# Performance work log

Hardware: AMD Instinct MI355X
Metric: run time of the kernel (lower is better)

Reference implementation:

```python
import jax, jax.numpy as jnp
import numpy as np

B, T = 1, 2048
N_EMBD = 4096
N_HEAD = 32
N_GROUPS = 8
HEAD = 128
Q_PER_KV = N_HEAD // N_GROUPS  # 4
WINDOW = 1024
EPS = 1e-5
ROPE_THETA = 10000.0


def setup_inputs() -> dict:
    key = jax.random.key(0)
    k0, k1, k2 = jax.random.split(key, 3)
    x = jax.random.normal(k0, (B, T, N_EMBD), dtype=jnp.float32)
    # RoPE tables: cos/sin of shape [T, HEAD] (rotary_percentage=1.0)
    inv_freq = 1.0 / (ROPE_THETA ** (jnp.arange(0, HEAD, 2, dtype=jnp.float32) / HEAD))
    ang = jnp.arange(T, dtype=jnp.float32)[:, None] * inv_freq[None, :]  # [T, HEAD//2]
    ang = jnp.concatenate([ang, ang], axis=-1)  # [T, HEAD]
    cos, sin = jnp.cos(ang), jnp.sin(ang)
    qkv_out = (N_HEAD + 2 * N_GROUPS) * HEAD  # 6144
    W_qkv = jax.random.normal(k1, (qkv_out, N_EMBD), dtype=jnp.float32) * 0.02
    W_proj = jax.random.normal(k2, (N_EMBD, N_HEAD * HEAD), dtype=jnp.float32) * 0.02
    norm_q_w = jnp.ones((N_HEAD * HEAD,), dtype=jnp.float32)
    norm_k_w = jnp.ones((N_GROUPS * HEAD,), dtype=jnp.float32)
    return {"x": x, "cos": cos, "sin": sin, "W_qkv": W_qkv,
            "norm_q_w": norm_q_w, "norm_k_w": norm_k_w, "W_proj": W_proj}


def _rmsnorm(x, w):
    # RMSNorm over last dim, matching litgpt RMSNorm (eps inside sqrt)
    var = jnp.mean(x * x, axis=-1, keepdims=True)
    return x * jax.lax.rsqrt(var + EPS) * w


def _apply_rope(x, cos, sin):
    # x: [B, H, T, D]; cos/sin: [T, D] (broadcast over B, H)
    d = x.shape[-1]
    x1, x2 = x[..., : d // 2], x[..., d // 2:]
    rotated = jnp.concatenate([-x2, x1], axis=-1)
    return x * cos + rotated * sin


def reference(x, cos, sin, W_qkv, norm_q_w, norm_k_w, W_proj):
    Bx, Tx, _ = x.shape
    qkv = jnp.einsum('btc,oc->bto', x, W_qkv)  # [B, T, (H+2G)*D]
    q_size = N_HEAD * HEAD
    kv_size = N_GROUPS * HEAD
    q = qkv[..., :q_size]
    k = qkv[..., q_size:q_size + kv_size]
    v = qkv[..., q_size + kv_size:]
    # norm_qk: RMSNorm over the full flattened q / k dims (pre head reshape)
    q = _rmsnorm(q, norm_q_w)
    k = _rmsnorm(k, norm_k_w)
    q = q.reshape(Bx, Tx, N_HEAD, HEAD).transpose(0, 2, 1, 3)     # [B, H, T, D]
    k = k.reshape(Bx, Tx, N_GROUPS, HEAD).transpose(0, 2, 1, 3)   # [B, G, T, D]
    v = v.reshape(Bx, Tx, N_GROUPS, HEAD).transpose(0, 2, 1, 3)   # [B, G, T, D]
    # rope_n_elem == head_size (rotary_percentage = 1.0)
    q = _apply_rope(q, cos, sin)
    k = _apply_rope(k, cos, sin)
    # GQA: expand kv groups to heads (repeat_interleave on head dim)
    k = jnp.repeat(k, Q_PER_KV, axis=1)  # [B, H, T, D]
    v = jnp.repeat(v, Q_PER_KV, axis=1)
    scale = 1.0 / jnp.sqrt(jnp.float32(HEAD))  # attention_scores_scalar is None
    scores = jnp.einsum('bhqd,bhkd->bhqk', q, k) * scale
    # causal + sliding-window mask: allowed iff 0 <= q_idx - kv_idx < WINDOW
    d = jnp.arange(Tx)[:, None] - jnp.arange(Tx)[None, :]
    bias = jnp.where((d >= 0) & (d < WINDOW), 0.0, -jnp.inf).astype(scores.dtype)
    attn = jax.nn.softmax(scores + bias, axis=-1)
    y = jnp.einsum('bhqk,bhkd->bhqd', attn, v)        # [B, H, T, D]
    y = y.transpose(0, 2, 1, 3).reshape(Bx, Tx, N_HEAD * HEAD)
    return jnp.einsum('bth,oh->bto', y, W_proj)       # [B, T, n_embd]
```

## Files before the change

kernel.cpp:

```cpp
#include <hip/hip_runtime.h>
#include <stdint.h>
#include <stddef.h>

#define T_SEQ 2048
#define WINDOW_SZ 1024

typedef __attribute__((ext_vector_type(4))) float f32x4;
typedef __attribute__((ext_vector_type(16))) float f32x16;
typedef __attribute__((ext_vector_type(8))) short s16x8;
typedef __attribute__((ext_vector_type(4))) short s16x4;

__device__ inline unsigned short f2bf(float f) {
  union { float f; unsigned u; } v; v.f = f;
  unsigned u = v.u;
  return (unsigned short)((u + 0x7fffu + ((u >> 16) & 1u)) >> 16);
}
__device__ inline float bf2f(unsigned short u) {
  union { unsigned u; float f; } v; v.u = ((unsigned)u) << 16; return v.f;
}

__device__ inline void gld_lds16(const unsigned short* g, unsigned short* l) {
  __builtin_amdgcn_global_load_lds((const __attribute__((address_space(1))) void*)g,
                                   (__attribute__((address_space(3))) void*)l, 16, 0, 0);
}

__device__ inline void store_out(float* p, float v) { *p = v; }
__device__ inline void store_out(unsigned short* p, float v) { *p = f2bf(v); }

__global__ __launch_bounds__(256) void cvt_all(const float* __restrict__ x,
                                               const float* __restrict__ wqkv,
                                               const float* __restrict__ wproj,
                                               unsigned short* __restrict__ x_bf,
                                               unsigned short* __restrict__ wqkv_bf,
                                               unsigned short* __restrict__ wproj_bf) {
  int i = blockIdx.x * 256 + threadIdx.x;
  const float* s; unsigned short* d; int j;
  if (i < 2097152)       { s = x;     d = x_bf;     j = i; }
  else if (i < 8388608)  { s = wqkv;  d = wqkv_bf;  j = i - 2097152; }
  else                   { s = wproj; d = wproj_bf; j = i - 8388608; }
  float4 v = ((const float4*)s)[j];
  ushort4 o;
  o.x = f2bf(v.x); o.y = f2bf(v.y); o.z = f2bf(v.z); o.w = f2bf(v.w);
  ((ushort4*)d)[j] = o;
}

template <typename OutT>
__global__ __launch_bounds__(256) void gemm_bt(const unsigned short* __restrict__ A,
                                               const unsigned short* __restrict__ Bt,
                                               OutT* __restrict__ C, int M, int N, int K) {
  __shared__ unsigned short As[128 * 64];
  __shared__ unsigned short Bs[128 * 64];
  const int tid  = threadIdx.x;
  const int wave = tid >> 6, lane = tid & 63;
  const int l32 = lane & 31, khalf = lane >> 5;
  const int m0 = blockIdx.y << 7, n0 = blockIdx.x << 7;
  const int wr = (wave >> 1) << 6;
  const int wc = (wave & 1) << 6;
  const int srow = wave * 8 + (lane >> 3);
  const int gchunk0 = lane & 7;

  f32x16 acc[2][2] = {};

  for (int k0 = 0; k0 < K; k0 += 64) {
#pragma unroll
    for (int j = 0; j < 4; j++) {
      int r = j * 32 + srow;
      int gc = gchunk0 ^ (r & 7);
      gld_lds16(A  + (size_t)(m0 + r) * K + k0 + gc * 8, &As[(j * 32 + wave * 8) * 64]);
      gld_lds16(Bt + (size_t)(n0 + r) * K + k0 + gc * 8, &Bs[(j * 32 + wave * 8) * 64]);
    }
    __syncthreads();
#pragma unroll
    for (int s = 0; s < 4; s++) {
      s16x8 af[2], bfr[2];
      int chunk = s * 2 + khalf;
#pragma unroll
      for (int i = 0; i < 2; i++) {
        int ra = wr + i * 32 + l32;
        af[i]  = *(const s16x8*)&As[ra * 64 + ((chunk ^ (ra & 7)) * 8)];
        int rb = wc + i * 32 + l32;
        bfr[i] = *(const s16x8*)&Bs[rb * 64 + ((chunk ^ (rb & 7)) * 8)];
      }
#pragma unroll
      for (int mi = 0; mi < 2; mi++)
#pragma unroll
        for (int ni = 0; ni < 2; ni++)
          acc[mi][ni] = __builtin_amdgcn_mfma_f32_32x32x16_bf16(af[mi], bfr[ni], acc[mi][ni], 0, 0, 0);
    }
    __syncthreads();
  }
#pragma unroll
  for (int mi = 0; mi < 2; mi++)
#pragma unroll
    for (int ni = 0; ni < 2; ni++) {
      int col = n0 + wc + ni * 32 + l32;
      int rbase = m0 + wr + mi * 32 + 4 * khalf;
#pragma unroll
      for (int reg = 0; reg < 16; reg++) {
        int row = rbase + (reg & 3) + 8 * (reg >> 2);
        store_out(&C[(size_t)row * N + col], acc[mi][ni][reg]);
      }
    }
}

__device__ inline void stage_half(const unsigned short* __restrict__ g, int ldk,
                                  int grow0, int k0, unsigned short* lds,
                                  int wave, int lane) {
#pragma unroll
  for (int j = 0; j < 2; j++) {
    int rloc = j * 64 + wave * 8 + (lane >> 3);
    int lc = (lane & 7) ^ (rloc & 7);
    gld_lds16(g + (size_t)(grow0 + rloc) * ldk + k0 + lc * 8,
              lds + (j * 64 + wave * 8) * 64);
  }
}
__device__ inline void stage_64(const unsigned short* __restrict__ g, int ldk,
                                int grow0, int k0, unsigned short* lds,
                                int wave, int lane) {
  int rloc = wave * 8 + (lane >> 3);
  int lc = (lane & 7) ^ (rloc & 7);
  gld_lds16(g + (size_t)(grow0 + rloc) * ldk + k0 + lc * 8,
            lds + (wave * 8) * 64);
}

__global__ __launch_bounds__(512, 2) void gemm256(const unsigned short* __restrict__ A,
                                                  const unsigned short* __restrict__ Bt,
                                                  unsigned short* __restrict__ C,
                                                  int M, int N, int K) {
  __shared__ unsigned short S[57344];
  const int tid = threadIdx.x, wave = tid >> 6, lane = tid & 63;
  const int quad = lane >> 4, l16 = lane & 15;
  const int wm = wave >> 2, wn = wave & 3;
  const int m0 = blockIdx.y << 8, n0 = blockIdx.x * 192;
  const int NT = K >> 6;

  f32x4 acc[8][3] = {};

  stage_half(Bt, K, n0,       0, &S[16384],        wave, lane);
  stage_64  (Bt, K, n0 + 128, 0, &S[16384 + 8192], wave, lane);
  stage_half(A,  K, m0,       0, &S[0],            wave, lane);
  stage_half(A,  K, m0 + 128, 0, &S[8192],         wave, lane);
  if (NT > 1) {
    stage_half(Bt, K, n0,       64, &S[28672 + 16384],        wave, lane);
    stage_64  (Bt, K, n0 + 128, 64, &S[28672 + 16384 + 8192], wave, lane);
  }
  asm volatile("s_waitcnt vmcnt(3)" ::: "memory");
  __builtin_amdgcn_s_barrier();
  asm volatile("" ::: "memory");

  for (int u = 0; u < NT; ++u) {
    const int b = u & 1;
    const unsigned short* Sa = &S[b * 28672];
    const unsigned short* Sb = &S[b * 28672 + 16384];
    s16x8 bfr[3][2];
#pragma unroll
    for (int p = 0; p < 4; ++p) {
      s16x8 af[2][2];
#pragma unroll
      for (int f = 0; f < 2; f++)
#pragma unroll
        for (int ks = 0; ks < 2; ks++) {
          int ra = wm * 128 + (p * 2 + f) * 16 + l16;
          af[f][ks] = *(const s16x8*)&Sa[ra * 64 + (((ks * 4 + quad) ^ (ra & 7)) * 8)];
        }
      if (p == 0) {
#pragma unroll
        for (int nf = 0; nf < 3; nf++)
#pragma unroll
          for (int ks = 0; ks < 2; ks++) {
            int rb = wn * 48 + nf * 16 + l16;
            bfr[nf][ks] = *(const s16x8*)&Sb[rb * 64 + (((ks * 4 + quad) ^ (rb & 7)) * 8)];
          }
      }
      if (p == 0 && u + 1 < NT) stage_half(A,  K, m0,       (u + 1) << 6, &S[(b ^ 1) * 28672],        wave, lane);
      if (p == 1 && u + 1 < NT) stage_half(A,  K, m0 + 128, (u + 1) << 6, &S[(b ^ 1) * 28672 + 8192], wave, lane);
      if (p == 2 && u + 2 < NT) stage_half(Bt, K, n0,       (u + 2) << 6, &S[b * 28672 + 16384],      wave, lane);
      if (p == 3 && u + 2 < NT) stage_64  (Bt, K, n0 + 128, (u + 2) << 6, &S[b * 28672 + 24576],      wave, lane);

      asm volatile("" ::: "memory");
      __builtin_amdgcn_s_barrier();
      asm volatile("" ::: "memory");
      __builtin_amdgcn_s_setprio(1);
#pragma unroll
      for (int f = 0; f < 2; f++)
#pragma unroll
        for (int nf = 0; nf < 3; nf++)
#pragma unroll
          for (int ks = 0; ks < 2; ks++)
            acc[p * 2 + f][nf] = __builtin_amdgcn_mfma_f32_16x16x32_bf16(
                af[f][ks], bfr[nf][ks], acc[p * 2 + f][nf], 0, 0, 0);
      __builtin_amdgcn_s_setprio(0);
      if (p == 3) {
        if (u + 2 < NT) asm volatile("s_waitcnt vmcnt(3)" ::: "memory");
        else            asm volatile("s_waitcnt vmcnt(0)" ::: "memory");
      }
      asm volatile("" ::: "memory");
      __builtin_amdgcn_s_barrier();
      asm volatile("" ::: "memory");
    }
  }
#pragma unroll
  for (int mf = 0; mf < 8; mf++)
#pragma unroll
    for (int nf = 0; nf < 3; nf++) {
      const int row0 = m0 + wm * 128 + mf * 16 + quad * 4;
      const int col  = n0 + wn * 48 + nf * 16 + l16;
#pragma unroll
      for (int r = 0; r < 4; r++)
        C[(size_t)(row0 + r) * N + col] = f2bf(acc[mf][nf][r]);
    }
}

__global__ __launch_bounds__(256) void normrope(const unsigned short* __restrict__ qkv,
                                                const float* __restrict__ cosb,
                                                const float* __restrict__ sinb,
                                                const float* __restrict__ wq,
                                                const float* __restrict__ wk,
                                                unsigned short* __restrict__ qr,
                                                unsigned short* __restrict__ kr,
                                                unsigned short* __restrict__ vt) {
  const int t = blockIdx.x, tid = threadIdx.x;
  const unsigned short* row = qkv + (size_t)t * 6144;
  float sq = 0.f, sk = 0.f;
  {
    s16x8 a = *(const s16x8*)&row[tid * 16];
    s16x8 b = *(const s16x8*)&row[tid * 16 + 8];
#pragma unroll
    for (int j = 0; j < 8; j++) {
      float fa = bf2f((unsigned short)a[j]), fb = bf2f((unsigned short)b[j]);
      sq += fa * fa + fb * fb;
    }
  }
  {
    s16x4 a = *(const s16x4*)&row[4096 + tid * 4];
#pragma unroll
    for (int j = 0; j < 4; j++) {
      float fa = bf2f((unsigned short)a[j]);
      sk += fa * fa;
    }
  }
#pragma unroll
  for (int off = 32; off; off >>= 1) { sq += __shfl_xor(sq, off); sk += __shfl_xor(sk, off); }
  __shared__ float red[8];
  if ((tid & 63) == 0) { red[tid >> 6] = sq; red[4 + (tid >> 6)] = sk; }
  __syncthreads();
  sq = red[0] + red[1] + red[2] + red[3];
  sk = red[4] + red[5] + red[6] + red[7];
  const float rq = rsqrtf(sq * (1.f / 4096.f) + 1e-5f) * (0.08838834764831845f * 1.4426950408889634f);
  const float rk = rsqrtf(sk * (1.f / 1024.f) + 1e-5f);
  for (int i = tid; i < 4096; i += 256) {
    int h = i >> 7, d = i & 127;
    int pd = (d < 64) ? d + 64 : d - 64;
    float val = bf2f(row[i]) * rq * wq[i];
    float pv  = bf2f(row[(h << 7) + pd]) * rq * wq[(h << 7) + pd];
    float rot = (d < 64) ? -pv : pv;
    float o = val * cosb[t * 128 + d] + rot * sinb[t * 128 + d];
    qr[(size_t)h * T_SEQ * 128 + t * 128 + d] = f2bf(o);
  }
  for (int i = tid; i < 1024; i += 256) {
    int g = i >> 7, d = i & 127;
    int pd = (d < 64) ? d + 64 : d - 64;
    float val = bf2f(row[4096 + i]) * rk * wk[i];
    float pv  = bf2f(row[4096 + (g << 7) + pd]) * rk * wk[(g << 7) + pd];
    float rot = (d < 64) ? -pv : pv;
    float o = val * cosb[t * 128 + d] + rot * sinb[t * 128 + d];
    kr[(size_t)g * T_SEQ * 128 + t * 128 + d] = f2bf(o);
  }
  for (int i = tid; i < 1024; i += 256) {
    int g = i >> 7, d = i & 127;
    vt[(size_t)g * 128 * T_SEQ + (size_t)d * T_SEQ + t] = row[5120 + i];
  }
}

__global__ __launch_bounds__(512, 2) void attn(const unsigned short* __restrict__ Q,
                                               const unsigned short* __restrict__ Kb,
                                               const unsigned short* __restrict__ Vt,
                                               unsigned short* __restrict__ Y) {
  __shared__ unsigned short Kbuf[2][64 * 128];
  __shared__ unsigned short Vbuf[2][128 * 64];
  __shared__ unsigned short Pbuf[8][2][16 * 72];
  const int qb = blockIdx.x, g = blockIdx.y;
  const int tid = threadIdx.x, wave = tid >> 6, lane = tid & 63;
  const int quad = lane >> 4, l16 = lane & 15;
  const int h = g * 4 + (wave >> 1);
  const int qbase = qb * 64;
  const int q0 = qbase + (wave & 1) * 32;
  const unsigned short* Qh = Q + (size_t)h * T_SEQ * 128;
  const unsigned short* Kg = Kb + (size_t)g * T_SEQ * 128;
  const unsigned short* Vg = Vt + (size_t)g * 128 * T_SEQ;

  s16x8 aq[2][4];
#pragma unroll
  for (int qt = 0; qt < 2; qt++)
#pragma unroll
    for (int ks = 0; ks < 4; ks++)
      aq[qt][ks] = *(const s16x8*)&Qh[(size_t)(q0 + qt * 16 + l16) * 128 + ks * 32 + quad * 8];

  f32x4 acc[2][8] = {};
  float lrow[2][4] = {};

  int lo = qbase - (WINDOW_SZ - 1);
  if (lo < 0) lo = 0;
  lo &= ~63;

#define STAGE_CHUNK(buf, kkv)                                                        \
  {                                                                                  \
    int kk_ = (kkv);                                                                 \
    _Pragma("unroll")                                                                \
    for (int j = 0; j < 2; j++) {                                                    \
      int rloc = wave * 8 + j * 4 + (lane >> 4);                                     \
      int oct = (lane & 15) ^ (rloc & 15);                                           \
      gld_lds16(Kg + (size_t)(kk_ + rloc) * 128 + oct * 8,                           \
                &Kbuf[buf][(wave * 8 + j * 4) * 128]);                               \
    }                                                                                \
    _Pragma("unroll")                                                                \
    for (int j = 0; j < 2; j++) {                                                    \
      int dloc = wave * 16 + j * 8 + (lane >> 3);                                    \
      int oct = (lane & 7) ^ (dloc & 7);                                             \
      gld_lds16(Vg + (size_t)dloc * T_SEQ + kk_ + oct * 8,                           \
                &Vbuf[buf][(wave * 16 + j * 8) * 64]);                               \
    }                                                                                \
  }

  STAGE_CHUNK(0, lo);
  int ib = 0;
  for (int kk = lo; kk < qbase + 64; kk += 64, ib ^= 1) {
    __syncthreads();
    if (kk + 64 < qbase + 64) STAGE_CHUNK(ib ^ 1, kk + 64);
    if (kk > q0 + 31 || kk + 63 < q0 - (WINDOW_SZ - 1)) continue;
    const unsigned short* kb = Kbuf[ib];
    const unsigned short* vb = Vbuf[ib];
    f32x4 sc[2][4] = {};
    __builtin_amdgcn_s_setprio(1);
#pragma unroll
    for (int ks = 0; ks < 4; ks++) {
#pragma unroll
      for (int ci = 0; ci < 4; ci++) {
        s16x8 bk = *(const s16x8*)&kb[(ci * 16 + l16) * 128 + (((ks * 4 + quad) ^ l16) * 8)];
        sc[0][ci] = __builtin_amdgcn_mfma_f32_16x16x32_bf16(aq[0][ks], bk, sc[0][ci], 0, 0, 0);
        sc[1][ci] = __builtin_amdgcn_mfma_f32_16x16x32_bf16(aq[1][ks], bk, sc[1][ci], 0, 0, 0);
      }
    }
    __builtin_amdgcn_s_setprio(0);
#pragma unroll
    for (int qt = 0; qt < 2; qt++)
#pragma unroll
      for (int ci = 0; ci < 4; ci++) {
        int col = kk + ci * 16 + l16;
#pragma unroll
        for (int r = 0; r < 4; r++) {
          int irow = q0 + qt * 16 + quad * 4 + r;
          unsigned dd = (unsigned)(irow - col);
          float e = (dd < (unsigned)WINDOW_SZ) ? exp2f(sc[qt][ci][r]) : 0.f;
          lrow[qt][r] += e;
          Pbuf[wave][qt][(quad * 4 + r) * 72 + ci * 16 + l16] = f2bf(e);
        }
      }
    __builtin_amdgcn_s_setprio(1);
#pragma unroll
    for (int c = 0; c < 2; c++) {
      s16x8 pa0 = *(const s16x8*)&Pbuf[wave][0][l16 * 72 + c * 32 + quad * 8];
      s16x8 pa1 = *(const s16x8*)&Pbuf[wave][1][l16 * 72 + c * 32 + quad * 8];
#pragma unroll
      for (int n = 0; n < 8; n++) {
        s16x8 bv = *(const s16x8*)&vb[(n * 16 + l16) * 64 + (((c * 4 + quad) ^ (l16 & 7)) * 8)];
        acc[0][n] = __builtin_amdgcn_mfma_f32_16x16x32_bf16(pa0, bv, acc[0][n], 0, 0, 0);
        acc[1][n] = __builtin_amdgcn_mfma_f32_16x16x32_bf16(pa1, bv, acc[1][n], 0, 0, 0);
      }
    }
    __builtin_amdgcn_s_setprio(0);
  }
#undef STAGE_CHUNK
#pragma unroll
  for (int qt = 0; qt < 2; qt++)
#pragma unroll
    for (int r = 0; r < 4; r++) {
#pragma unroll
      for (int off = 8; off; off >>= 1) lrow[qt][r] += __shfl_xor(lrow[qt][r], off);
      lrow[qt][r] = 1.f / lrow[qt][r];
    }
#pragma unroll
  for (int qt = 0; qt < 2; qt++)
#pragma unroll
    for (int n = 0; n < 8; n++)
#pragma unroll
      for (int r = 0; r < 4; r++) {
        int irow = q0 + qt * 16 + quad * 4 + r;
        Y[(size_t)irow * 4096 + h * 128 + n * 16 + l16] = f2bf(acc[qt][n][r] * lrow[qt][r]);
      }
}

extern "C" void kernel_launch(void* const* d_in, const int* in_sizes, int n_in,
                              void* d_out, int out_size, void* d_ws, size_t ws_size,
                              hipStream_t stream) {
  (void)in_sizes; (void)n_in; (void)out_size; (void)ws_size;
  const float* x     = (const float*)d_in[0];
  const float* cosb  = (const float*)d_in[1];
  const float* sinb  = (const float*)d_in[2];
  const float* Wqkv  = (const float*)d_in[3];
  const float* wq    = (const float*)d_in[4];
  const float* wk    = (const float*)d_in[5];
  const float* Wproj = (const float*)d_in[6];
  float* out = (float*)d_out;

  char* ws = (char*)d_ws;
  unsigned short* x_bf     = (unsigned short*)(ws);
  unsigned short* wqkv_bf  = (unsigned short*)(ws + 16777216);
  unsigned short* wproj_bf = (unsigned short*)(ws + 67108864);
  unsigned short* qkv      = (unsigned short*)(ws + 100663296);
  unsigned short* qr       = (unsigned short*)(ws + 150994944);
  unsigned short* kr       = (unsigned short*)(ws + 167772160);
  unsigned short* vt       = (unsigned short*)(ws + 171966464);
  unsigned short* y        = (unsigned short*)(ws + 176160768);

  cvt_all<<<49152, 256, 0, stream>>>(x, Wqkv, Wproj, x_bf, wqkv_bf, wproj_bf);
  gemm256<<<dim3(32, 8), 512, 0, stream>>>(x_bf, wqkv_bf, qkv, 2048, 6144, 4096);
  normrope<<<2048, 256, 0, stream>>>(qkv, cosb, sinb, wq, wk, qr, kr, vt);
  attn<<<dim3(32, 8), 512, 0, stream>>>(qr, kr, vt, y);
  gemm_bt<float><<<dim3(32, 16), 256, 0, stream>>>(y, wproj_bf, out, 2048, 4096, 4096);
}
```

Before: 480.0 us.

## Triple-buffer A tiles in GEMM LDS to prefetch two K-steps ahead

The bf16 GEMM kernel now gives the A operand three LDS buffers instead of two. It prefetches both A and B two K-iterations ahead, and relaxes the vmcnt waits to match the larger number of loads in flight. Before, A was fetched only one step ahead, so its global-load latency was less hidden than B's. The cost is a bigger shared-memory footprint per block, about 144 KB, plus extra rotating-index bookkeeping. The old layout already exceeded two blocks per CU, so occupancy should be unchanged.

Result: no change. 479.9 us (-0.0%).

```diff
diff --git a/kernel.cpp b/kernel.cpp
--- a/kernel.cpp
+++ b/kernel.cpp
@@ -127,7 +127,7 @@
                                                   const unsigned short* __restrict__ Bt,
                                                   unsigned short* __restrict__ C,
                                                   int M, int N, int K) {
-  __shared__ unsigned short S[57344];
+  __shared__ unsigned short S[73728];
   const int tid = threadIdx.x, wave = tid >> 6, lane = tid & 63;
   const int quad = lane >> 4, l16 = lane & 15;
   const int wm = wave >> 2, wn = wave & 3;
@@ -136,22 +136,32 @@
 
   f32x4 acc[8][3] = {};
 
-  stage_half(Bt, K, n0,       0, &S[16384],        wave, lane);
-  stage_64  (Bt, K, n0 + 128, 0, &S[16384 + 8192], wave, lane);
-  stage_half(A,  K, m0,       0, &S[0],            wave, lane);
-  stage_half(A,  K, m0 + 128, 0, &S[8192],         wave, lane);
+  unsigned short* const Ab0 = &S[0];
+  unsigned short* const Bb0 = &S[49152];
+
+  stage_half(A,  K, m0,       0, Ab0,        wave, lane);
+  stage_half(A,  K, m0 + 128, 0, Ab0 + 8192, wave, lane);
+  stage_half(Bt, K, n0,       0, Bb0,        wave, lane);
+  stage_64  (Bt, K, n0 + 128, 0, Bb0 + 8192, wave, lane);
   if (NT > 1) {
-    stage_half(Bt, K, n0,       64, &S[28672 + 16384],        wave, lane);
-    stage_64  (Bt, K, n0 + 128, 64, &S[28672 + 16384 + 8192], wave, lane);
-  }
-  asm volatile("s_waitcnt vmcnt(3)" ::: "memory");
+    stage_half(A,  K, m0,       64, Ab0 + 16384,        wave, lane);
+    stage_half(A,  K, m0 + 128, 64, Ab0 + 16384 + 8192, wave, lane);
+    stage_half(Bt, K, n0,       64, Bb0 + 12288,        wave, lane);
+    stage_64  (Bt, K, n0 + 128, 64, Bb0 + 12288 + 8192, wave, lane);
+    asm volatile("s_waitcnt vmcnt(7)" ::: "memory");
+  } else {
+    asm volatile("s_waitcnt vmcnt(0)" ::: "memory");
+  }
   __builtin_amdgcn_s_barrier();
   asm volatile("" ::: "memory");
 
+  int ac = 0;
   for (int u = 0; u < NT; ++u) {
-    const int b = u & 1;
-    const unsigned short* Sa = &S[b * 28672];
-    const unsigned short* Sb = &S[b * 28672 + 16384];
+    const unsigned short* Sa = Ab0 + ac * 16384;
+    const unsigned short* Sb = Bb0 + (u & 1) * 12288;
+    int an2 = ac + 2; if (an2 >= 3) an2 -= 3;
+    unsigned short* SaN = Ab0 + an2 * 16384;
+    unsigned short* SbN = Bb0 + (u & 1) * 12288;
     s16x8 bfr[3][2];
 #pragma unroll
     for (int p = 0; p < 4; ++p) {
@@ -172,10 +182,10 @@
             bfr[nf][ks] = *(const s16x8*)&Sb[rb * 64 + (((ks * 4 + quad) ^ (rb & 7)) * 8)];
           }
       }
-      if (p == 0 && u + 1 < NT) stage_half(A,  K, m0,       (u + 1) << 6, &S[(b ^ 1) * 28672],        wave, lane);
-      if (p == 1 && u + 1 < NT) stage_half(A,  K, m0 + 128, (u + 1) << 6, &S[(b ^ 1) * 28672 + 8192], wave, lane);
-      if (p == 2 && u + 2 < NT) stage_half(Bt, K, n0,       (u + 2) << 6, &S[b * 28672 + 16384],      wave, lane);
-      if (p == 3 && u + 2 < NT) stage_64  (Bt, K, n0 + 128, (u + 2) << 6, &S[b * 28672 + 24576],      wave, lane);
+      if (p == 0 && u + 2 < NT) stage_half(A,  K, m0,       (u + 2) << 6, SaN,        wave, lane);
+      if (p == 1 && u + 2 < NT) stage_half(A,  K, m0 + 128, (u + 2) << 6, SaN + 8192, wave, lane);
+      if (p == 2 && u + 2 < NT) stage_half(Bt, K, n0,       (u + 2) << 6, SbN,        wave, lane);
+      if (p == 3 && u + 2 < NT) stage_64  (Bt, K, n0 + 128, (u + 2) << 6, SbN + 8192, wave, lane);
 
       asm volatile("" ::: "memory");
       __builtin_amdgcn_s_barrier();
@@ -191,13 +201,14 @@
                 af[f][ks], bfr[nf][ks], acc[p * 2 + f][nf], 0, 0, 0);
       __builtin_amdgcn_s_setprio(0);
       if (p == 3) {
-        if (u + 2 < NT) asm volatile("s_waitcnt vmcnt(3)" ::: "memory");
+        if (u + 2 < NT) asm volatile("s_waitcnt vmcnt(7)" ::: "memory");
         else            asm volatile("s_waitcnt vmcnt(0)" ::: "memory");
       }
       asm volatile("" ::: "memory");
       __builtin_amdgcn_s_barrier();
       asm volatile("" ::: "memory");
     }
+    ac = (ac == 2) ? 0 : ac + 1;
   }
 #pragma unroll
   for (int mf = 0; mf < 8; mf++)
```
